# Kernel optimization log

Measured on AMD Instinct MI355X. Metric: run time of the kernel, lower is better.

The kernel has to match this reference:

```python
import jax, jax.numpy as jnp
import numpy as np

N = 100000   # nodes
E = 1600000  # edges
G = 256      # graphs
NF = 7       # node features
EF = 3       # edge features (in/out)
UD = 2       # global feature dim
H = 128      # hidden dim
NL = 2       # MetaLayers = n_layers - 1
DOUT = 1


def _lin_init(k, fan_in, fan_out):
    return jax.random.normal(k, (fan_in, fan_out), jnp.float32) / np.sqrt(fan_in)


def _mlp2(h, W1, b1, W2, b2):
    return jax.nn.relu(h @ W1 + b1) @ W2 + b2


def setup_inputs() -> dict:
    key = jax.random.key(0)
    ks = jax.random.split(key, 40)
    x = jax.random.normal(ks[0], (N, NF), jnp.float32)
    edge_index = jax.random.randint(ks[1], (2, E), 0, N, jnp.int64)
    edge_attr = jax.random.normal(ks[2], (E, EF), jnp.float32)
    u = jax.random.normal(ks[3], (G, UD), jnp.float32)
    batch = jnp.sort(jax.random.randint(ks[4], (N,), 0, G, jnp.int64))
    # stacked per-layer params (NL identical layers)
    e_in = 2 * NF + EF          # 17
    n_in = NF + 3 * EF + UD     # 18
    eW1 = jnp.stack([_lin_init(ks[5 + i], e_in, H) for i in range(NL)])
    eb1 = jnp.zeros((NL, H), jnp.float32)
    eW2 = jnp.stack([_lin_init(ks[7 + i], H, EF) for i in range(NL)])
    eb2 = jnp.zeros((NL, EF), jnp.float32)
    nW1 = jnp.stack([_lin_init(ks[9 + i], n_in, H) for i in range(NL)])
    nb1 = jnp.zeros((NL, H), jnp.float32)
    nW2 = jnp.stack([_lin_init(ks[11 + i], H, NF) for i in range(NL)])
    nb2 = jnp.zeros((NL, NF), jnp.float32)
    # output head: 3*node_out + global_in -> H -> H -> H -> dim_out
    oW1 = _lin_init(ks[20], 3 * NF + UD, H); ob1 = jnp.zeros((H,), jnp.float32)
    oW2 = _lin_init(ks[21], H, H); ob2 = jnp.zeros((H,), jnp.float32)
    oW3 = _lin_init(ks[22], H, H); ob3 = jnp.zeros((H,), jnp.float32)
    oW4 = _lin_init(ks[23], H, DOUT); ob4 = jnp.zeros((DOUT,), jnp.float32)
    return dict(x=x, edge_attr=edge_attr, u=u,
                eW1=eW1, eb1=eb1, eW2=eW2, eb2=eb2,
                nW1=nW1, nb1=nb1, nW2=nW2, nb2=nb2,
                oW1=oW1, ob1=ob1, oW2=oW2, ob2=ob2,
                oW3=oW3, ob3=ob3, oW4=oW4, ob4=ob4,
                edge_index=edge_index, batch=batch)


def _segment_reduce3(vals, seg, num):
    # add / max (empty -> 0, matching torch_scatter fill) / mean
    s = jax.ops.segment_sum(vals, seg, num_segments=num)
    cnt = jax.ops.segment_sum(jnp.ones((vals.shape[0], 1), vals.dtype), seg, num_segments=num)
    m = jax.ops.segment_max(vals, seg, num_segments=num)
    m = jnp.where(cnt > 0, m, jnp.zeros_like(m))
    mean = s / jnp.maximum(cnt, 1.0)
    return s, m, mean, cnt


def reference(x, edge_attr, u, eW1, eb1, eW2, eb2, nW1, nb1, nW2, nb2,
              oW1, ob1, oW2, ob2, oW3, ob3, oW4, ob4, edge_index, batch):
    row, col = edge_index[0], edge_index[1]
    for l in range(NL):
        # EdgeModel: gather src/dest node feats + edge feats -> MLP
        e_in = jnp.concatenate([x[row], x[col], edge_attr], axis=1)  # [E, 2*NF+EF]
        edge_attr = _mlp2(e_in, eW1[l], eb1[l], eW2[l], eb2[l])      # [E, EF]
        # NodeModel: three scatter reductions over incoming edges (col)
        s, m, mean, _ = _segment_reduce3(edge_attr, col, N)
        n_in = jnp.concatenate([x, s, m, mean, u[batch]], axis=1)    # [N, NF+3*EF+UD]
        x = _mlp2(n_in, nW1[l], nb1[l], nW2[l], nb2[l])              # [N, NF]
    # global pools per graph
    s, m, mean, _ = _segment_reduce3(x, batch, G)
    h = jnp.concatenate([s, mean, m, u], axis=1)                     # [G, 3*NF+UD]
    h = jax.nn.relu(h @ oW1 + ob1)
    h = jax.nn.relu(h @ oW2 + ob2)
    h = jax.nn.relu(h @ oW3 + ob3)
    return h @ oW4 + ob4                                             # [G, DOUT]
```

## Files before the change

### kernel.cpp

```cpp
#include <hip/hip_runtime.h>

#define NN 100000
#define NE 1600000
#define NG 256
#define NB 391
#define NBH 1024
#define CHUNK 1563
#define NBINS 1024
#define NBUCK 782

typedef __attribute__((ext_vector_type(8))) short short8v;
typedef __attribute__((ext_vector_type(4))) float float4v;

__device__ __forceinline__ unsigned short f2bf(float f) {
    unsigned u = __float_as_uint(f);
    return (unsigned short)((u + 0x7FFFu + ((u >> 16) & 1u)) >> 16);
}

__global__ __launch_bounds__(256) void hist_kernel(
    const int* __restrict__ col, unsigned* __restrict__ ghist) {
    __shared__ unsigned h[NBINS];
    int b = blockIdx.x;
    for (int i = threadIdx.x; i < NBINS; i += 256) h[i] = 0;
    __syncthreads();
    int e0 = b * CHUNK;
    int e1 = e0 + CHUNK; if (e1 > NE) e1 = NE;
    for (int e = e0 + threadIdx.x; e < e1; e += 256)
        atomicAdd(&h[col[e] >> 7], 1u);
    __syncthreads();
    for (int i = threadIdx.x; i < NBINS; i += 256)
        ghist[(size_t)b * NBINS + i] = h[i];
}

__global__ __launch_bounds__(1024) void scanB_kernel(
    const unsigned* __restrict__ ghist, unsigned* __restrict__ goff,
    unsigned* __restrict__ total) {
    __shared__ unsigned a[NBH], bb[NBH];
    int bin = blockIdx.x, t = threadIdx.x;
    unsigned v = ghist[(size_t)t * NBINS + bin];
    a[t] = v;
    __syncthreads();
    unsigned* src = a; unsigned* dst = bb;
    for (int off = 1; off < NBH; off <<= 1) {
        unsigned x = src[t];
        if (t >= off) x += src[t - off];
        dst[t] = x;
        __syncthreads();
        unsigned* tmp = src; src = dst; dst = tmp;
    }
    goff[(size_t)t * NBINS + bin] = src[t] - v;
    if (t == NBH - 1) total[bin] = src[t];
}

__global__ __launch_bounds__(1024) void scanC_kernel(
    const unsigned* __restrict__ total, unsigned* __restrict__ binbase) {
    __shared__ unsigned a[NBINS], bb[NBINS];
    int t = threadIdx.x;
    unsigned v = total[t];
    a[t] = v;
    __syncthreads();
    unsigned* src = a; unsigned* dst = bb;
    for (int off = 1; off < NBINS; off <<= 1) {
        unsigned x = src[t];
        if (t >= off) x += src[t - off];
        dst[t] = x;
        __syncthreads();
        unsigned* tmp = src; src = dst; dst = tmp;
    }
    binbase[t] = src[t] - v;
    if (t == NBINS - 1) binbase[NBINS] = src[t];
}

__global__ __launch_bounds__(256) void scatterD_kernel(
    const int* __restrict__ row, const int* __restrict__ col,
    const float* __restrict__ ea,
    const unsigned* __restrict__ goff, const unsigned* __restrict__ binbase,
    int2* __restrict__ rcT, float* __restrict__ eabT) {
    __shared__ unsigned cur[NBINS];
    int b = blockIdx.x;
    for (int i = threadIdx.x; i < NBINS; i += 256) cur[i] = 0;
    __syncthreads();
    int e0 = b * CHUNK;
    int e1 = e0 + CHUNK; if (e1 > NE) e1 = NE;
    const unsigned* grow = goff + (size_t)b * NBINS;
    for (int e = e0 + threadIdx.x; e < e1; e += 256) {
        int c = col[e];
        int bin = c >> 7;
        unsigned l = atomicAdd(&cur[bin], 1u);
        unsigned slot = binbase[bin] + grow[bin] + l;
        rcT[slot] = make_int2(row[e], c);
        eabT[(size_t)slot * 3 + 0] = ea[(size_t)e * 3 + 0];
        eabT[(size_t)slot * 3 + 1] = ea[(size_t)e * 3 + 1];
        eabT[(size_t)slot * 3 + 2] = ea[(size_t)e * 3 + 2];
    }
}

__global__ __launch_bounds__(256) void bucketsort_kernel(
    const int2* __restrict__ rcT, const float* __restrict__ eabT,
    const unsigned* __restrict__ binbase,
    int2* __restrict__ rc, float* __restrict__ eab, unsigned* __restrict__ start)
{
    __shared__ unsigned lcnt[128], sa[128], sb[128], lcur[128];
    int bin = blockIdx.x, tid = threadIdx.x;
    if (tid < 128) lcnt[tid] = 0;
    __syncthreads();
    unsigned beg = binbase[bin], end = binbase[bin + 1];
    for (unsigned k = beg + tid; k < end; k += 256)
        atomicAdd(&lcnt[rcT[k].y & 127], 1u);
    __syncthreads();
    if (tid < 128) sa[tid] = lcnt[tid];
    __syncthreads();
    unsigned* src = sa; unsigned* dst = sb;
    for (int off = 1; off < 128; off <<= 1) {
        if (tid < 128) {
            unsigned v = src[tid];
            if (tid >= off) v += src[tid - off];
            dst[tid] = v;
        }
        __syncthreads();
        unsigned* t2 = src; src = dst; dst = t2;
    }
    if (tid < 128) {
        unsigned excl = src[tid] - lcnt[tid];
        lcur[tid] = excl;
        int n = (bin << 7) + tid;
        if (n < NN) {
            start[n] = beg + excl;
            if (n == NN - 1) start[NN] = beg + excl + lcnt[tid];
        }
    }
    __syncthreads();
    for (unsigned k = beg + tid; k < end; k += 256) {
        int2 p = rcT[k];
        unsigned l = atomicAdd(&lcur[p.y & 127], 1u);
        unsigned slot = beg + l;
        rc[slot] = p;
        eab[(size_t)slot * 3 + 0] = eabT[(size_t)k * 3 + 0];
        eab[(size_t)slot * 3 + 1] = eabT[(size_t)k * 3 + 1];
        eab[(size_t)slot * 3 + 2] = eabT[(size_t)k * 3 + 2];
    }
}

__global__ __launch_bounds__(256) void gbound_kernel(
    const int* __restrict__ batch, int* __restrict__ gstart) {
    int n = blockIdx.x * 256 + threadIdx.x;
    if (n >= NN) return;
    int b = batch[n];
    int bp = (n == 0) ? -1 : batch[n - 1];
    for (int g = bp + 1; g <= b; ++g) gstart[g] = n;
    if (n == NN - 1) {
        for (int g = b + 1; g <= NG; ++g) gstart[g] = NN;
    }
}

__global__ __launch_bounds__(256) void prep_kernel(
    const float* __restrict__ eW1, const float* __restrict__ eb1, const float* __restrict__ eW2,
    const float* __restrict__ nW1, const float* __restrict__ nb1, const float* __restrict__ nW2,
    short* __restrict__ ewf, float* __restrict__ w2f, float* __restrict__ b1f,
    float* __restrict__ nwt)
{
    int t = blockIdx.x * 256 + threadIdx.x;
    const int EWF = 2 * 4096;
    const int W2F = 2 * 1536;
    const int B1F = 2 * 512;
    const int NWT = 2 * 128 * 28;
    if (t < EWF) {
        int layer = t >> 12, r = t & 4095;
        int tt = r >> 9, r2 = r & 511;
        int l = r2 >> 3, i = r2 & 7;
        int kk = ((l >> 4) << 3) + i;
        int n = tt * 16 + (l & 15);
        float v = (kk < 17) ? eW1[layer * 17 * 128 + kk * 128 + n] : 0.f;
        ewf[t] = (short)f2bf(v);
    } else if (t < EWF + W2F) {
        int q = t - EWF;
        int layer = q / 1536, r = q % 1536;
        int l = r / 24, r2 = r % 24;
        int tt = r2 / 3, c = r2 % 3;
        int k = tt * 16 + (l & 15);
        w2f[q] = eW2[layer * 384 + k * 3 + c];
    } else if (t < EWF + W2F + B1F) {
        int q = t - EWF - W2F;
        int layer = q / 512, r = q % 512;
        int l = r / 8, tt = r % 8;
        b1f[q] = eb1[layer * 128 + tt * 16 + (l & 15)];
    } else if (t < EWF + W2F + B1F + NWT) {
        int q = t - EWF - W2F - B1F;
        int l = q / (128 * 28), rest = q % (128 * 28), j = rest / 28, i = rest % 28;
        float v = 0.f;
        if (i < 18)       v = nW1[l * 18 * 128 + i * 128 + j];
        else if (i == 18) v = nb1[l * 128 + j];
        else if (i < 26)  v = nW2[l * 128 * 7 + j * 7 + (i - 19)];
        nwt[q] = v;
    }
}

__global__ __launch_bounds__(256) void edge_kernel(
    const float* __restrict__ x, float* eab,
    const int2* __restrict__ rc,
    const short* __restrict__ ewf, const float* __restrict__ w2f,
    const float* __restrict__ b1f, const float* __restrict__ b2)
{
    int lane = threadIdx.x & 63;
    int l15 = lane & 15, lg = lane >> 4;
    int wid = (blockIdx.x * 256 + threadIdx.x) >> 6;
    int nwaves = gridDim.x * 4;

    short8v B1[8];
    #pragma unroll
    for (int t = 0; t < 8; ++t)
        B1[t] = *(const short8v*)(ewf + (t * 64 + lane) * 8);
    float w2a[8], w2b[8], w2c[8], b1v[8];
    #pragma unroll
    for (int t = 0; t < 8; ++t) {
        w2a[t] = w2f[lane * 24 + t * 3 + 0];
        w2b[t] = w2f[lane * 24 + t * 3 + 1];
        w2c[t] = w2f[lane * 24 + t * 3 + 2];
        b1v[t] = b1f[lane * 8 + t];
    }
    float bb0 = b2[0], bb1 = b2[1], bb2 = b2[2];

    const int NT = NE / 16;
    for (int tile = wid; tile < NT; tile += nwaves) {
        int s = tile * 16 + l15;
        int2 p = rc[s];
        const float* xr = x + (size_t)p.x * 7;
        const float* xc = x + (size_t)p.y * 7;
        const float* ep = eab + (size_t)s * 3;

        float av0 = 0.f, av1 = 0.f, av2 = 0.f, av3 = 0.f,
              av4 = 0.f, av5 = 0.f, av6 = 0.f, av7 = 0.f;
        if (lg == 0) {
            av0 = xr[0]; av1 = xr[1]; av2 = xr[2]; av3 = xr[3];
            av4 = xr[4]; av5 = xr[5]; av6 = xr[6]; av7 = xc[0];
        } else if (lg == 1) {
            av0 = xc[1]; av1 = xc[2]; av2 = xc[3]; av3 = xc[4];
            av4 = xc[5]; av5 = xc[6]; av6 = ep[0]; av7 = ep[1];
        } else if (lg == 2) {
            av0 = ep[2];
        }

        short8v A;
        A[0] = (short)f2bf(av0); A[1] = (short)f2bf(av1);
        A[2] = (short)f2bf(av2); A[3] = (short)f2bf(av3);
        A[4] = (short)f2bf(av4); A[5] = (short)f2bf(av5);
        A[6] = (short)f2bf(av6); A[7] = (short)f2bf(av7);

        float4v Z = {0.f, 0.f, 0.f, 0.f};
        float p00 = 0.f, p01 = 0.f, p02 = 0.f;
        float p10 = 0.f, p11 = 0.f, p12 = 0.f;
        float p20 = 0.f, p21 = 0.f, p22 = 0.f;
        float p30 = 0.f, p31 = 0.f, p32 = 0.f;

        #pragma unroll
        for (int g = 0; g < 2; ++g) {
            float4v C[4];
            #pragma unroll
            for (int q = 0; q < 4; ++q)
                C[q] = __builtin_amdgcn_mfma_f32_16x16x32_bf16(A, B1[g * 4 + q], Z, 0, 0, 0);
            #pragma unroll
            for (int q = 0; q < 4; ++q) {
                int t = g * 4 + q;
                float h0 = fmaxf(C[q][0] + b1v[t], 0.f);
                float h1 = fmaxf(C[q][1] + b1v[t], 0.f);
                float h2 = fmaxf(C[q][2] + b1v[t], 0.f);
                float h3 = fmaxf(C[q][3] + b1v[t], 0.f);
                p00 += h0 * w2a[t]; p01 += h0 * w2b[t]; p02 += h0 * w2c[t];
                p10 += h1 * w2a[t]; p11 += h1 * w2b[t]; p12 += h1 * w2c[t];
                p20 += h2 * w2a[t]; p21 += h2 * w2b[t]; p22 += h2 * w2c[t];
                p30 += h3 * w2a[t]; p31 += h3 * w2b[t]; p32 += h3 * w2c[t];
            }
        }
        #pragma unroll
        for (int m = 1; m < 16; m <<= 1) {
            p00 += __shfl_xor(p00, m, 16); p01 += __shfl_xor(p01, m, 16); p02 += __shfl_xor(p02, m, 16);
            p10 += __shfl_xor(p10, m, 16); p11 += __shfl_xor(p11, m, 16); p12 += __shfl_xor(p12, m, 16);
            p20 += __shfl_xor(p20, m, 16); p21 += __shfl_xor(p21, m, 16); p22 += __shfl_xor(p22, m, 16);
            p30 += __shfl_xor(p30, m, 16); p31 += __shfl_xor(p31, m, 16); p32 += __shfl_xor(p32, m, 16);
        }
        if (l15 < 4) {
            float o0 = (l15 == 0) ? p00 : (l15 == 1) ? p10 : (l15 == 2) ? p20 : p30;
            float o1 = (l15 == 0) ? p01 : (l15 == 1) ? p11 : (l15 == 2) ? p21 : p31;
            float o2 = (l15 == 0) ? p02 : (l15 == 1) ? p12 : (l15 == 2) ? p22 : p32;
            size_t off = (size_t)(tile * 16 + lg * 4 + l15) * 3;
            eab[off + 0] = o0 + bb0;
            eab[off + 1] = o1 + bb1;
            eab[off + 2] = o2 + bb2;
        }
    }
}

__global__ __launch_bounds__(256) void reduce_kernel(
    const float* __restrict__ eab, const unsigned* __restrict__ start,
    const float* __restrict__ u, const int* __restrict__ batch,
    float* __restrict__ nred)
{
    int gid = blockIdx.x * 256 + threadIdx.x;
    int n = gid >> 4, sub = gid & 15;
    if (n >= NN) return;
    unsigned sbeg = start[n], send = start[n + 1];

    float s0 = 0.f, s1 = 0.f, s2 = 0.f;
    float m0 = -__builtin_inff(), m1 = -__builtin_inff(), m2 = -__builtin_inff();
    for (unsigned k = sbeg + sub; k < send; k += 16) {
        float v0 = eab[(size_t)k * 3 + 0];
        float v1 = eab[(size_t)k * 3 + 1];
        float v2 = eab[(size_t)k * 3 + 2];
        s0 += v0; s1 += v1; s2 += v2;
        m0 = fmaxf(m0, v0); m1 = fmaxf(m1, v1); m2 = fmaxf(m2, v2);
    }
    #pragma unroll
    for (int msk = 1; msk < 16; msk <<= 1) {
        s0 += __shfl_xor(s0, msk, 16);
        s1 += __shfl_xor(s1, msk, 16);
        s2 += __shfl_xor(s2, msk, 16);
        m0 = fmaxf(m0, __shfl_xor(m0, msk, 16));
        m1 = fmaxf(m1, __shfl_xor(m1, msk, 16));
        m2 = fmaxf(m2, __shfl_xor(m2, msk, 16));
    }
    if (sub == 0) {
        float deg = (float)(send - sbeg);
        if (send == sbeg) { m0 = 0.f; m1 = 0.f; m2 = 0.f; }
        float inv = 1.f / fmaxf(deg, 1.f);
        int b = batch[n];
        float* o = nred + (size_t)n * 12;
        o[0] = s0; o[1] = s1; o[2] = s2;
        o[3] = m0; o[4] = m1; o[5] = m2;
        o[6] = s0 * inv; o[7] = s1 * inv; o[8] = s2 * inv;
        o[9] = u[b * 2 + 0]; o[10] = u[b * 2 + 1];
    }
}

#define NMLP_BLOCKS 1024
#define NMLP_WAVES (NMLP_BLOCKS * 4)
__global__ __launch_bounds__(256, 4) void nodemlp_kernel(
    const float* x_in, const float* __restrict__ nred,
    const float* __restrict__ wt, const float* __restrict__ b2,
    float* x_out)
{
    int lane = threadIdx.x & 63;
    int wid = (blockIdx.x * 256 + threadIdx.x) >> 6;

    const float* ra = wt + lane * 28;
    const float* rb = wt + (lane + 64) * 28;
    float a0 = ra[0], a1 = ra[1], a2 = ra[2], a3 = ra[3], a4 = ra[4], a5 = ra[5],
          a6 = ra[6], a7 = ra[7], a8 = ra[8], a9 = ra[9], a10 = ra[10], a11 = ra[11],
          a12 = ra[12], a13 = ra[13], a14 = ra[14], a15 = ra[15], a16 = ra[16], a17 = ra[17],
          ab = ra[18], p0 = ra[19], p1 = ra[20], p2 = ra[21], p3 = ra[22], p4 = ra[23],
          p5 = ra[24], p6 = ra[25];
    float b0 = rb[0], b1 = rb[1], b2_ = rb[2], b3 = rb[3], b4 = rb[4], b5 = rb[5],
          b6 = rb[6], b7 = rb[7], b8 = rb[8], b9 = rb[9], b10 = rb[10], b11 = rb[11],
          b12 = rb[12], b13 = rb[13], b14 = rb[14], b15 = rb[15], b16 = rb[16], b17 = rb[17],
          bb = rb[18], q0 = rb[19], q1 = rb[20], q2 = rb[21], q3 = rb[22], q4 = rb[23],
          q5 = rb[24], q6 = rb[25];

    asm volatile("" : "+v"(a0), "+v"(a1), "+v"(a2), "+v"(a3), "+v"(a4), "+v"(a5),
                      "+v"(a6), "+v"(a7), "+v"(a8), "+v"(a9), "+v"(a10), "+v"(a11),
                      "+v"(a12), "+v"(a13), "+v"(a14), "+v"(a15), "+v"(a16), "+v"(a17),
                      "+v"(ab), "+v"(p0), "+v"(p1), "+v"(p2), "+v"(p3), "+v"(p4),
                      "+v"(p5), "+v"(p6));
    asm volatile("" : "+v"(b0), "+v"(b1), "+v"(b2_), "+v"(b3), "+v"(b4), "+v"(b5),
                      "+v"(b6), "+v"(b7), "+v"(b8), "+v"(b9), "+v"(b10), "+v"(b11),
                      "+v"(b12), "+v"(b13), "+v"(b14), "+v"(b15), "+v"(b16), "+v"(b17),
                      "+v"(bb), "+v"(q0), "+v"(q1), "+v"(q2), "+v"(q3), "+v"(q4),
                      "+v"(q5), "+v"(q6));

    float B0 = b2[0], B1 = b2[1], B2 = b2[2], B3 = b2[3], B4 = b2[4], B5 = b2[5], B6 = b2[6];

    const int nper = (NN + NMLP_WAVES - 1) / NMLP_WAVES;
    int n0 = wid * nper;
    int n1 = n0 + nper; if (n1 > NN) n1 = NN;

    #pragma unroll 2
    for (int n = n0; n < n1; ++n) {
        int nu = __builtin_amdgcn_readfirstlane(n);
        const float* xp = x_in + (size_t)nu * 7;
        const float* rp = nred + (size_t)nu * 12;
        float i0 = xp[0], i1 = xp[1], i2 = xp[2], i3 = xp[3], i4 = xp[4], i5 = xp[5], i6 = xp[6];
        float s0 = rp[0], s1 = rp[1], s2 = rp[2];
        float m0 = rp[3], m1 = rp[4], m2 = rp[5];
        float e0 = rp[6], e1 = rp[7], e2 = rp[8];
        float u0 = rp[9], u1 = rp[10];

        float ha = ab, hb = bb;
        ha += i0 * a0;  hb += i0 * b0;
        ha += i1 * a1;  hb += i1 * b1;
        ha += i2 * a2;  hb += i2 * b2_;
        ha += i3 * a3;  hb += i3 * b3;
        ha += i4 * a4;  hb += i4 * b4;
        ha += i5 * a5;  hb += i5 * b5;
        ha += i6 * a6;  hb += i6 * b6;
        ha += s0 * a7;  hb += s0 * b7;
        ha += s1 * a8;  hb += s1 * b8;
        ha += s2 * a9;  hb += s2 * b9;
        ha += m0 * a10; hb += m0 * b10;
        ha += m1 * a11; hb += m1 * b11;
        ha += m2 * a12; hb += m2 * b12;
        ha += e0 * a13; hb += e0 * b13;
        ha += e1 * a14; hb += e1 * b14;
        ha += e2 * a15; hb += e2 * b15;
        ha += u0 * a16; hb += u0 * b16;
        ha += u1 * a17; hb += u1 * b17;
        ha = fmaxf(ha, 0.f); hb = fmaxf(hb, 0.f);

        float c0 = ha * p0 + hb * q0;
        float c1 = ha * p1 + hb * q1;
        float c2 = ha * p2 + hb * q2;
        float c3 = ha * p3 + hb * q3;
        float c4 = ha * p4 + hb * q4;
        float c5 = ha * p5 + hb * q5;
        float c6 = ha * p6 + hb * q6;
        #pragma unroll
        for (int msk = 1; msk < 64; msk <<= 1) {
            c0 += __shfl_xor(c0, msk);
            c1 += __shfl_xor(c1, msk);
            c2 += __shfl_xor(c2, msk);
            c3 += __shfl_xor(c3, msk);
            c4 += __shfl_xor(c4, msk);
            c5 += __shfl_xor(c5, msk);
            c6 += __shfl_xor(c6, msk);
        }
        float o = c0 + B0;
        if (lane == 1) o = c1 + B1;
        if (lane == 2) o = c2 + B2;
        if (lane == 3) o = c3 + B3;
        if (lane == 4) o = c4 + B4;
        if (lane == 5) o = c5 + B5;
        if (lane == 6) o = c6 + B6;
        if (lane < 7) x_out[(size_t)nu * 7 + lane] = o;
    }
}

__global__ __launch_bounds__(256) void pool_head_kernel(
    const float* __restrict__ x, const int* __restrict__ gstart,
    const float* __restrict__ u,
    const float* __restrict__ oW1, const float* __restrict__ ob1,
    const float* __restrict__ oW2, const float* __restrict__ ob2,
    const float* __restrict__ oW3, const float* __restrict__ ob3,
    const float* __restrict__ oW4, const float* __restrict__ ob4,
    float* __restrict__ out)
{
    int g = blockIdx.x, tid = threadIdx.x;
    int lane = tid & 63, wv = tid >> 6;
    int gs = gstart[g], ge = gstart[g + 1];

    float s0 = 0.f, s1 = 0.f, s2 = 0.f, s3 = 0.f, s4 = 0.f, s5 = 0.f, s6 = 0.f;
    float m0 = -__builtin_inff(), m1 = m0, m2 = m0, m3 = m0, m4 = m0, m5 = m0, m6 = m0;
    for (int n = gs + tid; n < ge; n += 256) {
        const float* xp = x + (size_t)n * 7;
        float v0 = xp[0], v1 = xp[1], v2 = xp[2], v3 = xp[3], v4 = xp[4], v5 = xp[5], v6 = xp[6];
        s0 += v0; s1 += v1; s2 += v2; s3 += v3; s4 += v4; s5 += v5; s6 += v6;
        m0 = fmaxf(m0, v0); m1 = fmaxf(m1, v1); m2 = fmaxf(m2, v2); m3 = fmaxf(m3, v3);
        m4 = fmaxf(m4, v4); m5 = fmaxf(m5, v5); m6 = fmaxf(m6, v6);
    }
    #pragma unroll
    for (int msk = 1; msk < 64; msk <<= 1) {
        s0 += __shfl_xor(s0, msk); s1 += __shfl_xor(s1, msk); s2 += __shfl_xor(s2, msk);
        s3 += __shfl_xor(s3, msk); s4 += __shfl_xor(s4, msk); s5 += __shfl_xor(s5, msk);
        s6 += __shfl_xor(s6, msk);
        m0 = fmaxf(m0, __shfl_xor(m0, msk)); m1 = fmaxf(m1, __shfl_xor(m1, msk));
        m2 = fmaxf(m2, __shfl_xor(m2, msk)); m3 = fmaxf(m3, __shfl_xor(m3, msk));
        m4 = fmaxf(m4, __shfl_xor(m4, msk)); m5 = fmaxf(m5, __shfl_xor(m5, msk));
        m6 = fmaxf(m6, __shfl_xor(m6, msk));
    }
    __shared__ float red[4][14];
    __shared__ float hin[23];
    __shared__ float ha[128];
    __shared__ float hbuf[128];
    if (lane == 0) {
        red[wv][0] = s0; red[wv][1] = s1; red[wv][2] = s2; red[wv][3] = s3;
        red[wv][4] = s4; red[wv][5] = s5; red[wv][6] = s6;
        red[wv][7] = m0; red[wv][8] = m1; red[wv][9] = m2; red[wv][10] = m3;
        red[wv][11] = m4; red[wv][12] = m5; red[wv][13] = m6;
    }
    __syncthreads();
    if (tid < 7) {
        float S = red[0][tid] + red[1][tid] + red[2][tid] + red[3][tid];
        float M = fmaxf(fmaxf(red[0][7 + tid], red[1][7 + tid]),
                        fmaxf(red[2][7 + tid], red[3][7 + tid]));
        float cntf = (float)(ge - gs);
        if (ge == gs) M = 0.f;
        hin[tid] = S;
        hin[7 + tid] = S / fmaxf(cntf, 1.f);
        hin[14 + tid] = M;
    }
    if (tid < 2) hin[21 + tid] = u[g * 2 + tid];
    __syncthreads();

    float h = 0.f;
    if (tid < 128) {
        h = ob1[tid];
        for (int i = 0; i < 23; ++i) h += hin[i] * oW1[i * 128 + tid];
        ha[tid] = fmaxf(h, 0.f);
    }
    __syncthreads();
    if (tid < 128) {
        h = ob2[tid];
        for (int i = 0; i < 128; ++i) h += ha[i] * oW2[i * 128 + tid];
        hbuf[tid] = fmaxf(h, 0.f);
    }
    __syncthreads();
    if (tid < 128) {
        h = ob3[tid];
        for (int i = 0; i < 128; ++i) h += hbuf[i] * oW3[i * 128 + tid];
        ha[tid] = fmaxf(h, 0.f) * oW4[tid];
    }
    __syncthreads();
    if (tid == 0) {
        float acc = ob4[0];
        for (int i = 0; i < 128; ++i) acc += ha[i];
        out[g] = acc;
    }
}

extern "C" void kernel_launch(void* const* d_in, const int* in_sizes, int n_in,
                              void* d_out, int out_size, void* d_ws, size_t ws_size,
                              hipStream_t stream) {
    const float* x         = (const float*)d_in[0];
    const float* edge_attr = (const float*)d_in[1];
    const float* u         = (const float*)d_in[2];
    const float* eW1 = (const float*)d_in[3];
    const float* eb1 = (const float*)d_in[4];
    const float* eW2 = (const float*)d_in[5];
    const float* eb2 = (const float*)d_in[6];
    const float* nW1 = (const float*)d_in[7];
    const float* nb1 = (const float*)d_in[8];
    const float* nW2 = (const float*)d_in[9];
    const float* nb2 = (const float*)d_in[10];
    const float* oW1 = (const float*)d_in[11];
    const float* ob1 = (const float*)d_in[12];
    const float* oW2 = (const float*)d_in[13];
    const float* ob2 = (const float*)d_in[14];
    const float* oW3 = (const float*)d_in[15];
    const float* ob3 = (const float*)d_in[16];
    const float* oW4 = (const float*)d_in[17];
    const float* ob4 = (const float*)d_in[18];
    const int* edge_index = (const int*)d_in[19];
    const int* batch      = (const int*)d_in[20];
    const int* row = edge_index;
    const int* col = edge_index + NE;

    float* ws        = (float*)d_ws;
    float* eab       = ws;
    float* eabT      = eab + (size_t)NE * 3;
    float* ws_x      = eabT + (size_t)NE * 3;
    int2*  rc        = (int2*)(ws_x + (size_t)NN * 7);
    int2*  rcT       = rc + (size_t)NE;
    float* nred      = (float*)(rcT + (size_t)NE);
    unsigned* ghist  = (unsigned*)(nred + (size_t)NN * 12);
    unsigned* goff   = ghist + (size_t)NBH * NBINS;
    unsigned* total  = goff + (size_t)NBH * NBINS;
    unsigned* binbase = total + NBINS;
    unsigned* startv = binbase + NBINS + 4;
    int* gstart      = (int*)(startv + NN + 4);
    float* nwt       = (float*)(gstart + 260);
    float* w2f       = nwt + 2 * 128 * 28;
    float* b1f       = w2f + 2 * 1536;
    uintptr_t ewb    = ((uintptr_t)(b1f + 2 * 512) + 15) & ~(uintptr_t)15;
    short* ewf       = (short*)ewb;

    dim3 b256(256);
    dim3 gn(NB);

    hist_kernel<<<NBH, b256, 0, stream>>>(col, ghist);
    gbound_kernel<<<gn, b256, 0, stream>>>(batch, gstart);
    scanB_kernel<<<NBINS, 1024, 0, stream>>>(ghist, goff, total);
    scanC_kernel<<<1, 1024, 0, stream>>>(total, binbase);
    scatterD_kernel<<<NBH, b256, 0, stream>>>(row, col, edge_attr, goff, binbase, rcT, eabT);
    bucketsort_kernel<<<NBUCK, b256, 0, stream>>>(rcT, eabT, binbase, rc, eab, startv);

    {
        int t = 2 * 4096 + 2 * 1536 + 2 * 512 + 2 * 128 * 28;
        prep_kernel<<<(t + 255) / 256, b256, 0, stream>>>(
            eW1, eb1, eW2, nW1, nb1, nW2, ewf, w2f, b1f, nwt);
    }

    dim3 gemf(2048);
    dim3 gr((NN * 16 + 255) / 256);

    edge_kernel<<<gemf, b256, 0, stream>>>(x, eab, rc, ewf, w2f, b1f, eb2);
    reduce_kernel<<<gr, b256, 0, stream>>>(eab, startv, u, batch, nred);
    nodemlp_kernel<<<NMLP_BLOCKS, b256, 0, stream>>>(x, nred, nwt, nb2, ws_x);

    edge_kernel<<<gemf, b256, 0, stream>>>(ws_x, eab, rc,
        ewf + 4096, w2f + 1536, b1f + 512, eb2 + 3);
    reduce_kernel<<<gr, b256, 0, stream>>>(eab, startv, u, batch, nred);
    nodemlp_kernel<<<NMLP_BLOCKS, b256, 0, stream>>>(ws_x, nred, nwt + 128 * 28, nb2 + 7, ws_x);

    pool_head_kernel<<<NG, b256, 0, stream>>>(ws_x, gstart, u,
        oW1, ob1, oW2, ob2, oW3, ob3, oW4, ob4, (float*)d_out);
}
```

Measured before the change: 395.0 us.

## Pad node and edge features to 8 and 4 floats for vector loads

Stores node features as 8-float rows and edge attributes as 4-float rows, so the edge kernel gathers them with 128-bit vector loads and the reduce kernel reads each edge with one float4 load. The edge weight matrix rows are remapped to match the new K layout (x_row 0-6, x_col 8-14, edge 16-18). A pad kernel converts the input x, and the node MLP and pool kernels are updated to the stride-8 layout. In exchange, edge-attribute memory traffic grows by a third and there is one extra small kernel launch.

```diff
diff --git a/kernel.cpp b/kernel.cpp
--- a/kernel.cpp
+++ b/kernel.cpp
@@ -98,7 +98,7 @@
 __global__ __launch_bounds__(256) void bucketsort_kernel(
     const int2* __restrict__ rcT, const float* __restrict__ eabT,
     const unsigned* __restrict__ binbase,
-    int2* __restrict__ rc, float* __restrict__ eab, unsigned* __restrict__ start)
+    int2* __restrict__ rc, float* __restrict__ eab4, unsigned* __restrict__ start)
 {
     __shared__ unsigned lcnt[128], sa[128], sb[128], lcur[128];
     int bin = blockIdx.x, tid = threadIdx.x;
@@ -135,9 +135,12 @@
         unsigned l = atomicAdd(&lcur[p.y & 127], 1u);
         unsigned slot = beg + l;
         rc[slot] = p;
-        eab[(size_t)slot * 3 + 0] = eabT[(size_t)k * 3 + 0];
-        eab[(size_t)slot * 3 + 1] = eabT[(size_t)k * 3 + 1];
-        eab[(size_t)slot * 3 + 2] = eabT[(size_t)k * 3 + 2];
+        float4v v;
+        v[0] = eabT[(size_t)k * 3 + 0];
+        v[1] = eabT[(size_t)k * 3 + 1];
+        v[2] = eabT[(size_t)k * 3 + 2];
+        v[3] = 0.f;
+        *(float4v*)(eab4 + (size_t)slot * 4) = v;
     }
 }
 
@@ -151,6 +154,19 @@
     if (n == NN - 1) {
         for (int g = b + 1; g <= NG; ++g) gstart[g] = NN;
     }
+}
+
+__global__ __launch_bounds__(256) void pad_kernel(
+    const float* __restrict__ x, float* __restrict__ x8) {
+    int n = blockIdx.x * 256 + threadIdx.x;
+    if (n >= NN) return;
+    float4v a, b;
+    a[0] = x[(size_t)n * 7 + 0]; a[1] = x[(size_t)n * 7 + 1];
+    a[2] = x[(size_t)n * 7 + 2]; a[3] = x[(size_t)n * 7 + 3];
+    b[0] = x[(size_t)n * 7 + 4]; b[1] = x[(size_t)n * 7 + 5];
+    b[2] = x[(size_t)n * 7 + 6]; b[3] = 0.f;
+    *(float4v*)(x8 + (size_t)n * 8 + 0) = a;
+    *(float4v*)(x8 + (size_t)n * 8 + 4) = b;
 }
 
 __global__ __launch_bounds__(256) void prep_kernel(
@@ -170,7 +186,11 @@
         int l = r2 >> 3, i = r2 & 7;
         int kk = ((l >> 4) << 3) + i;
         int n = tt * 16 + (l & 15);
-        float v = (kk < 17) ? eW1[layer * 17 * 128 + kk * 128 + n] : 0.f;
+        int orig = -1;
+        if (kk < 7)                   orig = kk;
+        else if (kk >= 8 && kk < 15)  orig = kk - 1;
+        else if (kk >= 16 && kk < 19) orig = kk - 2;
+        float v = (orig >= 0) ? eW1[layer * 17 * 128 + orig * 128 + n] : 0.f;
         ewf[t] = (short)f2bf(v);
     } else if (t < EWF + W2F) {
         int q = t - EWF;
@@ -196,7 +216,7 @@
 }
 
 __global__ __launch_bounds__(256) void edge_kernel(
-    const float* __restrict__ x, float* eab,
+    const float* __restrict__ x8, float* eab4,
     const int2* __restrict__ rc,
     const short* __restrict__ ewf, const float* __restrict__ w2f,
     const float* __restrict__ b1f, const float* __restrict__ b2)
@@ -224,27 +244,25 @@
     for (int tile = wid; tile < NT; tile += nwaves) {
         int s = tile * 16 + l15;
         int2 p = rc[s];
-        const float* xr = x + (size_t)p.x * 7;
-        const float* xc = x + (size_t)p.y * 7;
-        const float* ep = eab + (size_t)s * 3;
-
-        float av0 = 0.f, av1 = 0.f, av2 = 0.f, av3 = 0.f,
-              av4 = 0.f, av5 = 0.f, av6 = 0.f, av7 = 0.f;
+
+        float4v va = {0.f, 0.f, 0.f, 0.f};
+        float4v vb = {0.f, 0.f, 0.f, 0.f};
         if (lg == 0) {
-            av0 = xr[0]; av1 = xr[1]; av2 = xr[2]; av3 = xr[3];
-            av4 = xr[4]; av5 = xr[5]; av6 = xr[6]; av7 = xc[0];
+            va = *(const float4v*)(x8 + (size_t)p.x * 8 + 0);
+            vb = *(const float4v*)(x8 + (size_t)p.x * 8 + 4);
         } else if (lg == 1) {
-            av0 = xc[1]; av1 = xc[2]; av2 = xc[3]; av3 = xc[4];
-            av4 = xc[5]; av5 = xc[6]; av6 = ep[0]; av7 = ep[1];
+            va = *(const float4v*)(x8 + (size_t)p.y * 8 + 0);
+            vb = *(const float4v*)(x8 + (size_t)p.y * 8 + 4);
         } else if (lg == 2) {
-            av0 = ep[2];
+            va = *(const float4v*)(eab4 + (size_t)s * 4);
+            va[3] = 0.f;
         }
 
         short8v A;
-        A[0] = (short)f2bf(av0); A[1] = (short)f2bf(av1);
-        A[2] = (short)f2bf(av2); A[3] = (short)f2bf(av3);
-        A[4] = (short)f2bf(av4); A[5] = (short)f2bf(av5);
-        A[6] = (short)f2bf(av6); A[7] = (short)f2bf(av7);
+        A[0] = (short)f2bf(va[0]); A[1] = (short)f2bf(va[1]);
+        A[2] = (short)f2bf(va[2]); A[3] = (short)f2bf(va[3]);
+        A[4] = (short)f2bf(vb[0]); A[5] = (short)f2bf(vb[1]);
+        A[6] = (short)f2bf(vb[2]); A[7] = (short)f2bf(vb[3]);
 
         float4v Z = {0.f, 0.f, 0.f, 0.f};
         float p00 = 0.f, p01 = 0.f, p02 = 0.f;
@@ -282,16 +300,15 @@
             float o0 = (l15 == 0) ? p00 : (l15 == 1) ? p10 : (l15 == 2) ? p20 : p30;
             float o1 = (l15 == 0) ? p01 : (l15 == 1) ? p11 : (l15 == 2) ? p21 : p31;
             float o2 = (l15 == 0) ? p02 : (l15 == 1) ? p12 : (l15 == 2) ? p22 : p32;
-            size_t off = (size_t)(tile * 16 + lg * 4 + l15) * 3;
-            eab[off + 0] = o0 + bb0;
-            eab[off + 1] = o1 + bb1;
-            eab[off + 2] = o2 + bb2;
+            float4v ov;
+            ov[0] = o0 + bb0; ov[1] = o1 + bb1; ov[2] = o2 + bb2; ov[3] = 0.f;
+            *(float4v*)(eab4 + (size_t)(tile * 16 + lg * 4 + l15) * 4) = ov;
         }
     }
 }
 
 __global__ __launch_bounds__(256) void reduce_kernel(
-    const float* __restrict__ eab, const unsigned* __restrict__ start,
+    const float* __restrict__ eab4, const unsigned* __restrict__ start,
     const float* __restrict__ u, const int* __restrict__ batch,
     float* __restrict__ nred)
 {
@@ -303,11 +320,9 @@
     float s0 = 0.f, s1 = 0.f, s2 = 0.f;
     float m0 = -__builtin_inff(), m1 = -__builtin_inff(), m2 = -__builtin_inff();
     for (unsigned k = sbeg + sub; k < send; k += 16) {
-        float v0 = eab[(size_t)k * 3 + 0];
-        float v1 = eab[(size_t)k * 3 + 1];
-        float v2 = eab[(size_t)k * 3 + 2];
-        s0 += v0; s1 += v1; s2 += v2;
-        m0 = fmaxf(m0, v0); m1 = fmaxf(m1, v1); m2 = fmaxf(m2, v2);
+        float4v v = *(const float4v*)(eab4 + (size_t)k * 4);
+        s0 += v[0]; s1 += v[1]; s2 += v[2];
+        m0 = fmaxf(m0, v[0]); m1 = fmaxf(m1, v[1]); m2 = fmaxf(m2, v[2]);
     }
     #pragma unroll
     for (int msk = 1; msk < 16; msk <<= 1) {
@@ -374,7 +389,7 @@
     #pragma unroll 2
     for (int n = n0; n < n1; ++n) {
         int nu = __builtin_amdgcn_readfirstlane(n);
-        const float* xp = x_in + (size_t)nu * 7;
+        const float* xp = x_in + (size_t)nu * 8;
         const float* rp = nred + (size_t)nu * 12;
         float i0 = xp[0], i1 = xp[1], i2 = xp[2], i3 = xp[3], i4 = xp[4], i5 = xp[5], i6 = xp[6];
         float s0 = rp[0], s1 = rp[1], s2 = rp[2];
@@ -427,7 +442,8 @@
         if (lane == 4) o = c4 + B4;
         if (lane == 5) o = c5 + B5;
         if (lane == 6) o = c6 + B6;
-        if (lane < 7) x_out[(size_t)nu * 7 + lane] = o;
+        if (lane < 7) x_out[(size_t)nu * 8 + lane] = o;
+        if (lane == 7) x_out[(size_t)nu * 8 + 7] = 0.f;
     }
 }
 
@@ -447,7 +463,7 @@
     float s0 = 0.f, s1 = 0.f, s2 = 0.f, s3 = 0.f, s4 = 0.f, s5 = 0.f, s6 = 0.f;
     float m0 = -__builtin_inff(), m1 = m0, m2 = m0, m3 = m0, m4 = m0, m5 = m0, m6 = m0;
     for (int n = gs + tid; n < ge; n += 256) {
-        const float* xp = x + (size_t)n * 7;
+        const float* xp = x + (size_t)n * 8;
         float v0 = xp[0], v1 = xp[1], v2 = xp[2], v3 = xp[3], v4 = xp[4], v5 = xp[5], v6 = xp[6];
         s0 += v0; s1 += v1; s2 += v2; s3 += v3; s4 += v4; s5 += v5; s6 += v6;
         m0 = fmaxf(m0, v0); m1 = fmaxf(m1, v1); m2 = fmaxf(m2, v2); m3 = fmaxf(m3, v3);
@@ -541,10 +557,11 @@
     const int* col = edge_index + NE;
 
     float* ws        = (float*)d_ws;
-    float* eab       = ws;
-    float* eabT      = eab + (size_t)NE * 3;
-    float* ws_x      = eabT + (size_t)NE * 3;
-    int2*  rc        = (int2*)(ws_x + (size_t)NN * 7);
+    float* eab4      = ws;
+    float* eabT      = eab4 + (size_t)NE * 4;
+    float* x8_0      = eabT + (size_t)NE * 3;
+    float* xA8       = x8_0 + (size_t)NN * 8;
+    int2*  rc        = (int2*)(xA8 + (size_t)NN * 8);
     int2*  rcT       = rc + (size_t)NE;
     float* nred      = (float*)(rcT + (size_t)NE);
     unsigned* ghist  = (unsigned*)(nred + (size_t)NN * 12);
@@ -558,16 +575,18 @@
     float* b1f       = w2f + 2 * 1536;
     uintptr_t ewb    = ((uintptr_t)(b1f + 2 * 512) + 15) & ~(uintptr_t)15;
     short* ewf       = (short*)ewb;
+    float* xB8       = x8_0;
 
     dim3 b256(256);
     dim3 gn(NB);
 
     hist_kernel<<<NBH, b256, 0, stream>>>(col, ghist);
     gbound_kernel<<<gn, b256, 0, stream>>>(batch, gstart);
+    pad_kernel<<<gn, b256, 0, stream>>>(x, x8_0);
     scanB_kernel<<<NBINS, 1024, 0, stream>>>(ghist, goff, total);
     scanC_kernel<<<1, 1024, 0, stream>>>(total, binbase);
     scatterD_kernel<<<NBH, b256, 0, stream>>>(row, col, edge_attr, goff, binbase, rcT, eabT);
-    bucketsort_kernel<<<NBUCK, b256, 0, stream>>>(rcT, eabT, binbase, rc, eab, startv);
+    bucketsort_kernel<<<NBUCK, b256, 0, stream>>>(rcT, eabT, binbase, rc, eab4, startv);
 
     {
         int t = 2 * 4096 + 2 * 1536 + 2 * 512 + 2 * 128 * 28;
@@ -578,15 +597,16 @@
     dim3 gemf(2048);
     dim3 gr((NN * 16 + 255) / 256);
 
-    edge_kernel<<<gemf, b256, 0, stream>>>(x, eab, rc, ewf, w2f, b1f, eb2);
-    reduce_kernel<<<gr, b256, 0, stream>>>(eab, startv, u, batch, nred);
-    nodemlp_kernel<<<NMLP_BLOCKS, b256, 0, stream>>>(x, nred, nwt, nb2, ws_x);
-
-    edge_kernel<<<gemf, b256, 0, stream>>>(ws_x, eab, rc,
+    edge_kernel<<<gemf, b256, 0, stream>>>(x8_0, eab4, rc, ewf, w2f, b1f, eb2);
+    reduce_kernel<<<gr, b256, 0, stream>>>(eab4, startv, u, batch, nred);
+    nodemlp_kernel<<<NMLP_BLOCKS, b256, 0, stream>>>(x8_0, nred, nwt, nb2, xA8);
+
+    edge_kernel<<<gemf, b256, 0, stream>>>(xA8, eab4, rc,
         ewf + 4096, w2f + 1536, b1f + 512, eb2 + 3);
-    reduce_kernel<<<gr, b256, 0, stream>>>(eab, startv, u, batch, nred);
-    nodemlp_kernel<<<NMLP_BLOCKS, b256, 0, stream>>>(ws_x, nred, nwt + 128 * 28, nb2 + 7, ws_x);
-
-    pool_head_kernel<<<NG, b256, 0, stream>>>(ws_x, gstart, u,
+    reduce_kernel<<<gr, b256, 0, stream>>>(eab4, startv, u, batch, nred);
+    nodemlp_kernel<<<NMLP_BLOCKS, b256, 0, stream>>>(xA8, nred,
+        nwt + 128 * 28, nb2 + 7, xB8);
+
+    pool_head_kernel<<<NG, b256, 0, stream>>>(xB8, gstart, u,
         oW1, ob1, oW2, ob2, oW3, ob3, oW4, ob4, (float*)d_out);
 }
```

Measured after the change: 398.7 us. About the same (+0.9%).
